# Optimization experiments

Hardware: AMD Instinct MI355X
Metric: run time of the kernel (lower is better)

Reference implementation:

```python
import jax, jax.numpy as jnp
import numpy as np

# model constants
D = 2048; D_INNER = 4096; H = 64; P = 64; N = 128; K = 4; CHUNK = 256
E = 8; TOPK = 2; I_EXP = 1024; I_SH = 4096
EPS = 1e-5; RES_MULT = 0.22
CONV_DIM = D_INNER + 2 * N  # n_groups=1


def rmsnorm(x, w, eps=EPS):
    var = jnp.mean(x * x, axis=-1, keepdims=True)
    return x * jax.lax.rsqrt(var + eps) * w


def segsum(x):
    # x: [..., L] -> [..., L, L] lower-triangular cumulative sums, -inf above diag
    L = x.shape[-1]
    cs = jnp.cumsum(x, axis=-1)
    d = cs[..., :, None] - cs[..., None, :]
    mask = jnp.tril(jnp.ones((L, L), dtype=bool))
    return jnp.where(mask, d, -jnp.inf)


def ssd(x, dt, A, Bm, Cm, chunk=CHUNK):
    # x:[b,s,h,p] dt:[b,s,h] A:[h] Bm/Cm:[b,s,n] (single group)
    b, S, h, p = x.shape
    n = Bm.shape[-1]
    nc = S // chunk
    xc = x.reshape(b, nc, chunk, h, p)
    dtc = dt.reshape(b, nc, chunk, h)
    Bc = Bm.reshape(b, nc, chunk, n)
    Cc = Cm.reshape(b, nc, chunk, n)
    dA = jnp.transpose(dtc * A, (0, 1, 3, 2))          # [b,c,h,l]
    dA_cum = jnp.cumsum(dA, axis=-1)                    # [b,c,h,l]
    xdt = xc * dtc[..., None]                           # [b,c,l,h,p]
    # intra-chunk (quadratic attention-like block)
    CB = jnp.einsum('bcln,bcsn->bcls', Cc, Bc)
    Lmat = jnp.exp(segsum(dA))                          # [b,c,h,l,s]
    Y = jnp.einsum('bcls,bchls,bcshp->bclhp', CB, Lmat, xdt)
    # per-chunk final states
    decay_states = jnp.exp(dA_cum[..., -1:] - dA_cum)   # [b,c,h,l]
    states = jnp.einsum('bcln,bchl,bclhp->bchpn', Bc, decay_states, xdt)
    # inter-chunk recurrence (small scan over nc chunks)
    chunk_decay = jnp.exp(dA_cum[..., -1])              # [b,c,h]
    dec_c = jnp.moveaxis(chunk_decay, 1, 0)             # [c,b,h]
    st_c = jnp.moveaxis(states, 1, 0)                   # [c,b,h,p,n]

    def step(carry, inp):
        dec, st = inp
        return carry * dec[..., None, None] + st, carry

    _, prev = jax.lax.scan(step, jnp.zeros_like(st_c[0]), (dec_c, st_c))
    prev = jnp.moveaxis(prev, 0, 1)                     # [b,c,h,p,n] state before each chunk
    out_decay = jnp.exp(jnp.transpose(dA_cum, (0, 1, 3, 2)))  # [b,c,l,h]
    Y = Y + jnp.einsum('bcln,bchpn->bclhp', Cc, prev) * out_decay[..., None]
    return Y.reshape(b, S, h, p)


def causal_conv_silu(u, w, bias):
    # u:[b,s,c], depthwise causal conv kernel w:[c,K]
    S = u.shape[1]
    up = jnp.pad(u, ((0, 0), (K - 1, 0), (0, 0)))
    y = sum(up[:, i:i + S, :] * w[:, i] for i in range(K)) + bias
    return jax.nn.silu(y)


def setup_inputs() -> dict:
    key = jax.random.key(0)
    ks = jax.random.split(key, 16)
    B, S = 1, 4096
    sc = 0.02
    return {
        'positions': jnp.arange(B * S, dtype=jnp.int32).reshape(B, S),
        'hidden_states': jax.random.normal(ks[0], (B, S, D), jnp.float32),
        'ln1_w': jnp.ones((D,), jnp.float32),
        'in_proj_w': jax.random.normal(ks[1], (D, 2 * D_INNER + 2 * N + H), jnp.float32) * sc,
        'conv_w': jax.random.normal(ks[2], (CONV_DIM, K), jnp.float32) * 0.2,
        'conv_b': jnp.zeros((CONV_DIM,), jnp.float32),
        'A_log': jnp.log(jax.random.uniform(ks[3], (H,), jnp.float32, 1.0, 16.0)),
        'dt_bias': jax.random.normal(ks[4], (H,), jnp.float32) * 0.5,
        'D_param': jnp.ones((H,), jnp.float32),
        'mamba_norm_w': jnp.ones((D_INNER,), jnp.float32),
        'out_proj_w': jax.random.normal(ks[5], (D_INNER, D), jnp.float32) * sc,
        'ln2_w': jnp.ones((D,), jnp.float32),
        'router_w': jax.random.normal(ks[6], (D, E), jnp.float32) * sc,
        'moe_w_gate_up': jax.random.normal(ks[7], (E, D, 2 * I_EXP), jnp.float32) * sc,
        'moe_w_down': jax.random.normal(ks[8], (E, I_EXP, D), jnp.float32) * sc,
        'shared_w_in': jax.random.normal(ks[9], (D, 2 * I_SH), jnp.float32) * sc,
        'shared_w_out': jax.random.normal(ks[10], (I_SH, D), jnp.float32) * sc,
    }


def reference(positions, hidden_states, ln1_w, in_proj_w, conv_w, conv_b, A_log,
              dt_bias, D_param, mamba_norm_w, out_proj_w, ln2_w, router_w,
              moe_w_gate_up, moe_w_down, shared_w_in, shared_w_out):
    B, S, _ = hidden_states.shape
    residual = hidden_states
    h = rmsnorm(hidden_states, ln1_w)
    # ---- Mamba2 mixer ----
    proj = h @ in_proj_w                                  # [B,S,2*Di+2N+H]
    z = proj[..., :D_INNER]
    xBC = proj[..., D_INNER:D_INNER + CONV_DIM]
    dt_raw = proj[..., D_INNER + CONV_DIM:]
    xBC = causal_conv_silu(xBC, conv_w, conv_b)
    x = xBC[..., :D_INNER].reshape(B, S, H, P)
    Bm = xBC[..., D_INNER:D_INNER + N]
    Cm = xBC[..., D_INNER + N:]
    dt = jax.nn.softplus(dt_raw + dt_bias)                # [B,S,H]
    A = -jnp.exp(A_log)                                   # [H]
    y = ssd(x, dt, A, Bm, Cm) + x * D_param[None, None, :, None]
    y = y.reshape(B, S, D_INNER)
    y = rmsnorm(y * jax.nn.silu(z), mamba_norm_w)         # gated RMSNorm
    mamba_out = y @ out_proj_w
    hidden = residual + mamba_out * RES_MULT
    residual = hidden
    # ---- MoE + shared MLP ----
    h2 = rmsnorm(hidden, ln2_w)
    ht = h2.reshape(-1, D)
    T = ht.shape[0]
    logits = ht @ router_w                                # [T,E]
    topv, topi = jax.lax.top_k(logits, TOPK)
    wts = jax.nn.softmax(topv, axis=-1)
    gates = jnp.zeros((T, E), ht.dtype).at[jnp.arange(T)[:, None], topi].set(wts)
    moe_out = jnp.zeros_like(ht)
    for e in range(E):
        gu = ht @ moe_w_gate_up[e]
        a = jax.nn.silu(gu[:, :I_EXP]) * gu[:, I_EXP:]
        moe_out = moe_out + gates[:, e:e + 1] * (a @ moe_w_down[e])
    gu = ht @ shared_w_in
    shared_out = (jax.nn.silu(gu[:, :I_SH]) * gu[:, I_SH:]) @ shared_w_out
    ff = (moe_out + shared_out).reshape(B, S, D)
    hidden = residual + ff * RES_MULT
    return (hidden, residual)
```

## Files before the change

### kernel.cpp

```cpp
#include <hip/hip_runtime.h>
#include <stdint.h>

typedef unsigned short u16;
typedef __attribute__((ext_vector_type(8))) __bf16 bf16x8;
typedef __attribute__((ext_vector_type(4))) float f32x4;

#define SEQ     4096
#define DMODEL  2048
#define DINNER  4096
#define NHEADS  64
#define HEADP   64
#define NSTATE  128
#define NCHUNK  16
#define CHUNKL  256
#define NPROJ   8512
#define NPROJP  8576
#define CONVDIM 4352
#define RESM    0.22f
#define MAXROWS 9216
#define MAXTILE 72

static __device__ __forceinline__ u16 f2bf(float f){
  union { float f; uint32_t u; } v; v.f = f;
  uint32_t r = v.u + 0x7fffu + ((v.u >> 16) & 1u);
// ... 248 lines not shown
      for (int i = 0; i < 4; i++) {
        const float v = acc[mi][ni][i];
        const float vp = __shfl_xor(v, 1);
        if (!(fr & 1)) {
          const int m = m0 + wr * 64 + mi * 16 + g * 4 + i;
          aout[(size_t)m * Nhalf + (n >> 1)] = f2bf(siluf(v) * vp);
        }
      }
    }
  }
}

template<int EPI>
__global__ __launch_bounds__(256, 2) void gemm_dd(
    const u16* __restrict__ Ah, const u16* __restrict__ Al,
    const u16* __restrict__ Bh, const u16* __restrict__ Bl,
    float* __restrict__ Cf, const float* __restrict__ res,
    int Nreal, int K, int ldc, float alpha, int NB, int MB, int G)
{
  __shared__ u16 Ash[128 * 32];
  __shared__ u16 Asl[128 * 32];
  __shared__ u16 Bsh[128 * 32];
  __shared__ u16 Bsl[128 * 32];
  int bx, by; decode_tile(blockIdx.x, NB, MB, G, bx, by);
  const int tid = threadIdx.x, lane = tid & 63;
  const int wid = tid >> 6, wr = wid >> 1, wc = wid & 1;
  const int m0 = by * 128, n0 = bx * 128;
  const int fr = lane & 15, g = lane >> 4;
  const int sl8 = swz_rd_sl8(fr, g);
  const f32x4 zero = {0.f, 0.f, 0.f, 0.f};
  f32x4 acc[4][4];
  #pragma unroll
  for (int i = 0; i < 4; i++)
    #pragma unroll
    for (int j = 0; j < 4; j++) acc[i][j] = zero;
  const int c8 = swz_src_c8(tid);
  const size_t offA = (size_t)(m0 + (tid >> 2)) * K + c8;
  const size_t offB = (size_t)(n0 + (tid >> 2)) * K + c8;
  const size_t rstep = (size_t)64 * K;
  const int l0 = tid * 8;
  for (int k0 = 0; k0 < K; k0 += 32) {
    if (k0) __syncthreads();
    gll16(Ah + offA + k0,         &Ash[l0]);
    gll16(Ah + offA + k0 + rstep, &Ash[2048 + l0]);
    gll16(Al + offA + k0,         &Asl[l0]);
    gll16(Al + offA + k0 + rstep, &Asl[2048 + l0]);
    gll16(Bh + offB + k0,         &Bsh[l0]);
    gll16(Bh + offB + k0 + rstep, &Bsh[2048 + l0]);
    gll16(Bl + offB + k0,         &Bsl[l0]);
    gll16(Bl + offB + k0 + rstep, &Bsl[2048 + l0]);
    __syncthreads();
    bf16x8 ah[4], al[4], bh[4], bl[4];
    #pragma unroll
    for (int mi = 0; mi < 4; mi++) {
      const int a = (wr * 64 + mi * 16 + fr) * 32 + sl8;
      ah[mi] = *(const bf16x8*)&Ash[a];
      al[mi] = *(const bf16x8*)&Asl[a];
    }
    #pragma unroll
    for (int ni = 0; ni < 4; ni++) {
      const int b = (wc * 64 + ni * 16 + fr) * 32 + sl8;
      bh[ni] = *(const bf16x8*)&Bsh[b];
      bl[ni] = *(const bf16x8*)&Bsl[b];
    }
    #pragma unroll
    for (int mi = 0; mi < 4; mi++)
      #pragma unroll
      for (int ni = 0; ni < 4; ni++) {
        acc[mi][ni] = __builtin_amdgcn_mfma_f32_16x16x32_bf16(al[mi], bh[ni], acc[mi][ni], 0, 0, 0);
        acc[mi][ni] = __builtin_amdgcn_mfma_f32_16x16x32_bf16(ah[mi], bl[ni], acc[mi][ni], 0, 0, 0);
        acc[mi][ni] = __builtin_amdgcn_mfma_f32_16x16x32_bf16(ah[mi], bh[ni], acc[mi][ni], 0, 0, 0);
      }
  }
  #pragma unroll
  for (int mi = 0; mi < 4; mi++) {
    #pragma unroll
    for (int ni = 0; ni < 4; ni++) {
      const int n = n0 + wc * 64 + ni * 16 + fr;
      if (n >= Nreal) continue;
      #pragma unroll
      for (int i = 0; i < 4; i++) {
        const int m = m0 + wr * 64 + mi * 16 + g * 4 + i;
        const float v = acc[mi][ni][i];
        const size_t idx = (size_t)m * ldc + n;
        if constexpr (EPI == 1) {
          Cf[idx] = res[idx] + alpha * v;
        } else {
          Cf[idx] = v;
        }
      }
    }
  }
}

__global__ __launch_bounds__(256, 2) void gemm_moe_gu(
    const u16* __restrict__ ht, const u16* __restrict__ wGU,
    u16* __restrict__ abufp, const int* __restrict__ tokmap,
    const int* __restrict__ meta)
{
  const int by = blockIdx.y;
  if (by >= meta[24]) return;
  const int e = meta[32 + by];
  const int row0 = meta[104 + by];
  __shared__ u16 As[128 * 32];
  __shared__ u16 Bs[128 * 32];
  const int tid = threadIdx.x, lane = tid & 63;
  const int wid = tid >> 6, wr = wid >> 1, wc = wid & 1;
  const int n0 = blockIdx.x * 128;
  const int fr = lane & 15, g = lane >> 4;
  const int sl8 = swz_rd_sl8(fr, g);
  const f32x4 zero = {0.f, 0.f, 0.f, 0.f};
  f32x4 acc[4][4];
  #pragma unroll
  for (int i = 0; i < 4; i++)
    #pragma unroll
    for (int j = 0; j < 4; j++) acc[i][j] = zero;
  const int r4 = tid >> 2, c8 = swz_src_c8(tid);
  const int tok0 = tokmap[row0 + r4];
  const int tok1 = tokmap[row0 + 64 + r4];
  const u16* pA0 = ht + (size_t)tok0 * DMODEL + c8;
  const u16* pA1 = ht + (size_t)tok1 * DMODEL + c8;
  const u16* pB  = wGU + (size_t)e * 2048 * DMODEL + (size_t)(n0 + r4) * DMODEL + c8;
  const size_t rstep = (size_t)64 * DMODEL;
  const int l0 = tid * 8;
  for (int k0 = 0; k0 < DMODEL; k0 += 32) {
    if (k0) __syncthreads();
    gll16(pA0 + k0,        &As[l0]);
    gll16(pA1 + k0,        &As[2048 + l0]);
    gll16(pB + k0,         &Bs[l0]);
    gll16(pB + k0 + rstep, &Bs[2048 + l0]);
    __syncthreads();
    bf16x8 af[4], bfr[4];
    #pragma unroll
    for (int mi = 0; mi < 4; mi++)
      af[mi] = *(const bf16x8*)&As[(wr * 64 + mi * 16 + fr) * 32 + sl8];
    #pragma unroll
    for (int ni = 0; ni < 4; ni++)
      bfr[ni] = *(const bf16x8*)&Bs[(wc * 64 + ni * 16 + fr) * 32 + sl8];
    #pragma unroll
    for (int mi = 0; mi < 4; mi++)
      #pragma unroll
      for (int ni = 0; ni < 4; ni++)
        acc[mi][ni] = __builtin_amdgcn_mfma_f32_16x16x32_bf16(af[mi], bfr[ni], acc[mi][ni], 0, 0, 0);
  }
  #pragma unroll
  for (int mi = 0; mi < 4; mi++)
    #pragma unroll
    for (int ni = 0; ni < 4; ni++) {
      const int n = n0 + wc * 64 + ni * 16 + fr;
      #pragma unroll
      for (int i = 0; i < 4; i++) {
        const float v = acc[mi][ni][i];
        const float vp = __shfl_xor(v, 1);
        if (!(fr & 1)) {
          const int m = row0 + wr * 64 + mi * 16 + g * 4 + i;
          abufp[(size_t)m * 1024 + (n >> 1)] = f2bf(siluf(v) * vp);
        }
      }
    }
}

__global__ __launch_bounds__(256, 2) void gemm_moe_down(
    const u16* __restrict__ abuf, const u16* __restrict__ wDN,
    u16* __restrict__ dout, const float* __restrict__ gatew,
    const int* __restrict__ meta)
{
  const int by = blockIdx.y;
  if (by >= meta[24]) return;
  const int e = meta[32 + by];
  const int row0 = meta[104 + by];
  __shared__ u16 As[128 * 32];
  __shared__ u16 Bs[128 * 32];
  const int tid = threadIdx.x, lane = tid & 63;
  const int wid = tid >> 6, wr = wid >> 1, wc = wid & 1;
  const int n0 = blockIdx.x * 128;
  const int fr = lane & 15, g = lane >> 4;
  const int sl8 = swz_rd_sl8(fr, g);
  const f32x4 zero = {0.f, 0.f, 0.f, 0.f};
  f32x4 acc[4][4];
  #pragma unroll
  for (int i = 0; i < 4; i++)
    #pragma unroll
    for (int j = 0; j < 4; j++) acc[i][j] = zero;
  const int r4 = tid >> 2, c8 = swz_src_c8(tid);
  const u16* pA = abuf + (size_t)(row0 + r4) * 1024 + c8;
  const u16* pB = wDN + (size_t)e * 1024 * 2048 + (size_t)(n0 + r4) * 1024 + c8;
  const size_t rstepA = (size_t)64 * 1024;
  const int l0 = tid * 8;
  for (int k0 = 0; k0 < 1024; k0 += 32) {
    if (k0) __syncthreads();
    gll16(pA + k0,          &As[l0]);
    gll16(pA + k0 + rstepA, &As[2048 + l0]);
    gll16(pB + k0,          &Bs[l0]);
    gll16(pB + k0 + rstepA, &Bs[2048 + l0]);
    __syncthreads();
    bf16x8 af[4], bfr[4];
    #pragma unroll
    for (int mi = 0; mi < 4; mi++)
      af[mi] = *(const bf16x8*)&As[(wr * 64 + mi * 16 + fr) * 32 + sl8];
    #pragma unroll
    for (int ni = 0; ni < 4; ni++)
      bfr[ni] = *(const bf16x8*)&Bs[(wc * 64 + ni * 16 + fr) * 32 + sl8];
    #pragma unroll
    for (int mi = 0; mi < 4; mi++)
      #pragma unroll
      for (int ni = 0; ni < 4; ni++)
        acc[mi][ni] = __builtin_amdgcn_mfma_f32_16x16x32_bf16(af[mi], bfr[ni], acc[mi][ni], 0, 0, 0);
  }
  #pragma unroll
  for (int mi = 0; mi < 4; mi++)
    #pragma unroll
    for (int ni = 0; ni < 4; ni++) {
      const int n = n0 + wc * 64 + ni * 16 + fr;
      #pragma unroll
      for (int i = 0; i < 4; i++) {
        const int m = row0 + wr * 64 + mi * 16 + g * 4 + i;
        dout[(size_t)m * 2048 + n] = f2bf(acc[mi][ni][i] * gatew[m]);
      }
    }
}

__global__ __launch_bounds__(256) void conv_silu_dt(
    const float* __restrict__ proj, const float* __restrict__ cw, const float* __restrict__ cb,
    const float* __restrict__ dt_bias,
    float* __restrict__ x, float* __restrict__ Bc, float* __restrict__ Cc,
    float* __restrict__ dt)
{
  const int c = blockIdx.x * 256 + threadIdx.x;
  const int s = blockIdx.y;
  if (c < CONVDIM) {
    const float4 w = *(const float4*)&cw[c * 4];
    float acc = cb[c];
    const float* pc = proj + (size_t)DINNER + c;
    if (s >= 3) acc += pc[(size_t)(s-3) * NPROJP] * w.x;
    if (s >= 2) acc += pc[(size_t)(s-2) * NPROJP] * w.y;
    if (s >= 1) acc += pc[(size_t)(s-1) * NPROJP] * w.z;
    acc += pc[(size_t)s * NPROJP] * w.w;
    const float v = siluf(acc);
    if (c < DINNER)                 x[(size_t)s * DINNER + c] = v;
    else if (c < DINNER + NSTATE)   Bc[(size_t)s * NSTATE + (c - DINNER)] = v;
    else                            Cc[(size_t)s * NSTATE + (c - DINNER - NSTATE)] = v;
  } else if (c < CONVDIM + 64) {
    const int h = c - CONVDIM;
    const float v = proj[(size_t)s * NPROJP + (DINNER + CONVDIM) + h] + dt_bias[h];
    dt[(size_t)s * 64 + h] = fmaxf(v, 0.f) + log1pf(__expf(-fabsf(v)));
  }
}

__global__ __launch_bounds__(64) void ssd_cum_seq(
    const float* __restrict__ dt, const float* __restrict__ A_log,
    float* __restrict__ cum, float* __restrict__ cdec)
{
  const int c = blockIdx.x, h = threadIdx.x;
  const float A = -__expf(A_log[h]);
  float run = 0.f;
  float* co = cum + ((size_t)(c * 64 + h)) * 256;
  const float* dp = dt + (size_t)c * 256 * 64 + h;
  #pragma unroll 4
  for (int l = 0; l < 256; l++) {
    run += dp[(size_t)l * 64] * A;
    co[l] = run;
  }
  cdec[c * 64 + h] = __expf(run);
}

__global__ __launch_bounds__(256) void ssd_cb(
    const float* __restrict__ Cc, const float* __restrict__ Bc, float* __restrict__ CBt)
{
  const int c = blockIdx.y;
  const int lt = blockIdx.x >> 2, st = blockIdx.x & 3;
  if (st > lt) return;
  __shared__ float Cn[128][64];
  __shared__ float Bn[128][64];
  const int tid = threadIdx.x;
  #pragma unroll
  for (int rep = 0; rep < 8; rep++) {
    const int lin = rep * 1024 + tid * 4;
    const int r = lin >> 7, cc = lin & 127;
    float4 cv = *(const float4*)&Cc[((size_t)(c*256 + lt*64 + r)) * 128 + cc];
    float4 bv = *(const float4*)&Bc[((size_t)(c*256 + st*64 + r)) * 128 + cc];
    Cn[cc+0][r] = cv.x; Cn[cc+1][r] = cv.y; Cn[cc+2][r] = cv.z; Cn[cc+3][r] = cv.w;
    Bn[cc+0][r] = bv.x; Bn[cc+1][r] = bv.y; Bn[cc+2][r] = bv.z; Bn[cc+3][r] = bv.w;
  }
  __syncthreads();
  const int lb = (tid >> 4) * 4, sb = (tid & 15) * 4;
  float acc[4][4] = {};
  for (int n = 0; n < 128; n++) {
    float cv[4], bv[4];
    #pragma unroll
    for (int i = 0; i < 4; i++) { cv[i] = Cn[n][lb+i]; bv[i] = Bn[n][sb+i]; }
    #pragma unroll
    for (int i = 0; i < 4; i++)
      #pragma unroll
      for (int j = 0; j < 4; j++) acc[i][j] += cv[i] * bv[j];
  }
  #pragma unroll
  for (int is = 0; is < 4; is++) {
    const int sg = st*64 + sb + is;
    float4 o; o.x = acc[0][is]; o.y = acc[1][is]; o.z = acc[2][is]; o.w = acc[3][is];
    *(float4*)&CBt[((size_t)(c*256 + sg)) * 256 + lt*64 + lb] = o;
  }
}

__global__ __launch_bounds__(256, 2) void ssd_intra(
    const float* __restrict__ x, const float* __restrict__ dt, const float* __restrict__ cum,
    const float* __restrict__ CBt, float* __restrict__ Yw)
{
  const int c = blockIdx.x, h = blockIdx.y, l = threadIdx.x;
  __shared__ float xs[64][64];
  __shared__ float cumL[256];
  cumL[l] = cum[((size_t)(c*64 + h)) * 256 + l];
  float Y[64];
  #pragma unroll
  for (int p = 0; p < 64; p++) Y[p] = 0.f;
  const size_t cb0 = (size_t)c * 256 * 256;
  for (int st4 = 0; st4 < 4; st4++) {
    __syncthreads();
    {
      const int j = threadIdx.x >> 2, p0 = (threadIdx.x & 3) * 16;
      const int sg = c*256 + st4*64 + j;
      const float dtv = dt[(size_t)sg * 64 + h];
      const float* xr = x + (size_t)sg * DINNER + h*64 + p0;
      #pragma unroll
      for (int q4 = 0; q4 < 4; q4++) {
        const float4 v = *(const float4*)&xr[q4*4];
        xs[j][p0 + q4*4+0] = v.x * dtv;
        xs[j][p0 + q4*4+1] = v.y * dtv;
        xs[j][p0 + q4*4+2] = v.z * dtv;
        xs[j][p0 + q4*4+3] = v.w * dtv;
      }
    }
    __syncthreads();
    if (st4 * 64 <= l) {
      const float myc = cumL[l];
      const int smax = (64 < l - st4*64 + 1) ? 64 : (l - st4*64 + 1);
      for (int s = 0; s < smax; s++) {
        const int sg = st4*64 + s;
        const float coef = CBt[cb0 + (size_t)sg*256 + l] * __expf(myc - cumL[sg]);
        const float4* xr4 = (const float4*)&xs[s][0];
        #pragma unroll
        for (int p4 = 0; p4 < 16; p4++) {
          const float4 xv = xr4[p4];
          Y[p4*4+0] += coef * xv.x;
          Y[p4*4+1] += coef * xv.y;
          Y[p4*4+2] += coef * xv.z;
          Y[p4*4+3] += coef * xv.w;
        }
      }
    }
  }
  float* yo = Yw + (size_t)(c*256 + l) * DINNER + h*64;
  #pragma unroll
  for (int p4 = 0; p4 < 16; p4++) {
    float4 o; o.x = Y[p4*4+0]; o.y = Y[p4*4+1]; o.z = Y[p4*4+2]; o.w = Y[p4*4+3];
    *(float4*)&yo[p4*4] = o;
  }
}

__global__ __launch_bounds__(256, 2) void ssd_states(
    const float* __restrict__ x, const float* __restrict__ Bc, const float* __restrict__ dt,
    const float* __restrict__ cum, float* __restrict__ states)
{
  const int c = blockIdx.x, h = blockIdx.y;
  const int p = threadIdx.x >> 2, n0 = (threadIdx.x & 3) * 32;
  __shared__ float xl[64][64];
  __shared__ float Bl[64][128];
  __shared__ float cd[256];
  {
    const int l = threadIdx.x;
    const float* cumh = cum + ((size_t)(c*64 + h)) * 256;
    cd[l] = __expf(cumh[255] - cumh[l]) * dt[(size_t)(c*256 + l) * 64 + h];
  }
  float stv[32];
  #pragma unroll
  for (int q = 0; q < 32; q++) stv[q] = 0.f;
  for (int lt = 0; lt < 4; lt++) {
    __syncthreads();
    {
      const int j = threadIdx.x >> 2, p0 = (threadIdx.x & 3) * 16;
      const int sg = c*256 + lt*64 + j;
      const float* xr = x + (size_t)sg * DINNER + h*64 + p0;
      #pragma unroll
      for (int q4 = 0; q4 < 4; q4++)
        *(float4*)&xl[j][p0 + q4*4] = *(const float4*)&xr[q4*4];
    }
    #pragma unroll
    for (int rep = 0; rep < 8; rep++) {
      const int lin = rep * 1024 + threadIdx.x * 4;
      const int r = lin >> 7, cc = lin & 127;
      *(float4*)&Bl[r][cc] = *(const float4*)&Bc[((size_t)(c*256 + lt*64 + r)) * 128 + cc];
    }
    __syncthreads();
    for (int j = 0; j < 64; j++) {
      const float v = xl[j][p] * cd[lt*64 + j];
      const float4* br = (const float4*)&Bl[j][n0];
      #pragma unroll
      for (int q4 = 0; q4 < 8; q4++) {
        const float4 bv = br[q4];
        stv[q4*4+0] += v * bv.x;
        stv[q4*4+1] += v * bv.y;
        stv[q4*4+2] += v * bv.z;
        stv[q4*4+3] += v * bv.w;
      }
    }
  }
  float* so = states + (((size_t)(c*64 + h)) * 64 + p) * 128 + n0;
  #pragma unroll
  for (int q4 = 0; q4 < 8; q4++) {
    float4 o; o.x = stv[q4*4+0]; o.y = stv[q4*4+1]; o.z = stv[q4*4+2]; o.w = stv[q4*4+3];
    *(float4*)&so[q4*4] = o;
  }
}

__global__ void ssd_scan(
    const float* __restrict__ states, const float* __restrict__ cdec, float* __restrict__ prev)
{
  const int hp = blockIdx.x;
  const int n = threadIdx.x;
  const int h = hp >> 6;
  float carry = 0.f;
  for (int c = 0; c < NCHUNK; c++) {
    const size_t idx = ((size_t)c * 4096 + hp) * 128 + n;
    prev[idx] = carry;
    carry = carry * cdec[c*64 + h] + states[idx];
  }
}

__global__ __launch_bounds__(256, 2) void ssd_final(
    const float* __restrict__ Cc, const float* __restrict__ prev, const float* __restrict__ cum,
    const float* __restrict__ x, const float* __restrict__ proj, const float* __restrict__ Dp,
    float* __restrict__ Yw)
{
  const int c = blockIdx.x, h = blockIdx.y, l = threadIdx.x;
  __shared__ float pv[64][128];
  #pragma unroll
  for (int rep = 0; rep < 8; rep++) {
    const int lin = rep * 1024 + threadIdx.x * 4;
    const int p = lin >> 7, n = lin & 127;
    *(float4*)&pv[p][n] = *(const float4*)&prev[((size_t)c * 4096 + h*64 + p) * 128 + n];
  }
  __syncthreads();
  float acc[64];
  #pragma unroll
  for (int p = 0; p < 64; p++) acc[p] = 0.f;
  const float* ccrow = Cc + (size_t)(c*256 + l) * 128;
  for (int nt = 0; nt < 4; nt++) {
    float cr[32];
    #pragma unroll
    for (int j4 = 0; j4 < 8; j4++) {
      const float4 v = *(const float4*)&ccrow[nt*32 + j4*4];
      cr[j4*4+0] = v.x; cr[j4*4+1] = v.y; cr[j4*4+2] = v.z; cr[j4*4+3] = v.w;
    }
    #pragma unroll
    for (int p = 0; p < 64; p++) {
      const float4* pvp = (const float4*)&pv[p][nt*32];
      float s = 0.f;
      #pragma unroll
      for (int j4 = 0; j4 < 8; j4++) {
        const float4 b = pvp[j4];
        s += cr[j4*4+0]*b.x + cr[j4*4+1]*b.y + cr[j4*4+2]*b.z + cr[j4*4+3]*b.w;
      }
      acc[p] += s;
    }
  }
  const float odec = __expf(cum[((size_t)(c*64 + h)) * 256 + l]);
  const float Dv = Dp[h];
  const float* xr = x + (size_t)(c*256 + l) * DINNER + h*64;
  const float* zr = proj + (size_t)(c*256 + l) * NPROJP + h*64;
  float* yo = Yw + (size_t)(c*256 + l) * DINNER + h*64;
  #pragma unroll
  for (int p = 0; p < 64; p++) {
    const float yv = yo[p] + acc[p] * odec + Dv * xr[p];
    yo[p] = yv * siluf(zr[p]);
  }
}

__global__ __launch_bounds__(256) void router_norm(
    const float* __restrict__ h2, const float* __restrict__ ln2w,
    const float* __restrict__ rw, u16* __restrict__ ht,
    int* __restrict__ eidx, float* __restrict__ ew)
{
  const int t = blockIdx.x;
  const float* xr = h2 + (size_t)t * DMODEL;
  float ss = 0.f;
  for (int i = threadIdx.x * 4; i < DMODEL; i += 1024) {
    float4 v = *(const float4*)&xr[i];
    ss += v.x*v.x + v.y*v.y + v.z*v.z + v.w*v.w;
  }
  #pragma unroll
  for (int off = 32; off > 0; off >>= 1) ss += __shfl_down(ss, off);
  __shared__ float red[4];
  if ((threadIdx.x & 63) == 0) red[threadIdx.x >> 6] = ss;
  __syncthreads();
  const float scale = rsqrtf((red[0]+red[1]+red[2]+red[3]) / (float)DMODEL + 1e-5f);
  float acc[8];
  #pragma unroll
  for (int j = 0; j < 8; j++) acc[j] = 0.f;
  u16* o = ht + (size_t)t * DMODEL;
  for (int i = threadIdx.x; i < DMODEL; i += 256) {
    const float v = xr[i] * scale * ln2w[i];
    o[i] = f2bf(v);
    const float* r = rw + (size_t)i * 8;
    #pragma unroll
    for (int j = 0; j < 8; j++) acc[j] += v * r[j];
  }
  #pragma unroll
  for (int j = 0; j < 8; j++)
    #pragma unroll
    for (int off = 32; off > 0; off >>= 1) acc[j] += __shfl_down(acc[j], off);
  __shared__ float rbuf[4][8];
  if ((threadIdx.x & 63) == 0)
    #pragma unroll
    for (int j = 0; j < 8; j++) rbuf[threadIdx.x >> 6][j] = acc[j];
  __syncthreads();
  if (threadIdx.x == 0) {
    float lg[8];
    #pragma unroll
    for (int j = 0; j < 8; j++) lg[j] = rbuf[0][j]+rbuf[1][j]+rbuf[2][j]+rbuf[3][j];
    int i1 = 0;
    #pragma unroll
    for (int j = 1; j < 8; j++) if (lg[j] > lg[i1]) i1 = j;
    int i2 = -1;
    #pragma unroll
    for (int j = 0; j < 8; j++) if (j != i1 && (i2 < 0 || lg[j] > lg[i2])) i2 = j;
    const float e2 = __expf(lg[i2] - lg[i1]);
    const float inv = 1.f / (1.f + e2);
    eidx[t*2]   = i1;  ew[t*2]   = inv;
    eidx[t*2+1] = i2;  ew[t*2+1] = e2 * inv;
  }
}

__global__ void moe_zero(int* __restrict__ tokmap, int* __restrict__ meta)
{
  const int i = blockIdx.x * 256 + threadIdx.x;
  if (i < MAXROWS) tokmap[i] = 0;
  if (i < 16) meta[i] = 0;
}

__global__ void moe_count(const int* __restrict__ eidx, int* __restrict__ meta)
{
  const int i = blockIdx.x * 256 + threadIdx.x;
  if (i < SEQ * 2) atomicAdd(&meta[eidx[i]], 1);
}

__global__ void moe_offsets(int* __restrict__ meta)
{
  if (threadIdx.x != 0 || blockIdx.x != 0) return;
  int off = 0, T = 0;
  for (int e = 0; e < 8; e++) {
    meta[16 + e] = off;
    const int nt = (meta[e] + 127) >> 7;
    for (int j = 0; j < nt; j++) {
      meta[32 + T] = e;
      meta[104 + T] = off + j * 128;
      T++;
    }
    off += nt * 128;
  }
  meta[24] = T;
}

__global__ void moe_place(
    const int* __restrict__ eidx, const float* __restrict__ ew,
    int* __restrict__ meta, int* __restrict__ tokmap,
    float* __restrict__ gatew, int* __restrict__ posmap)
{
  const int i = blockIdx.x * 256 + threadIdx.x;
  if (i >= SEQ * 2) return;
  const int e = eidx[i];
  const int pos = atomicAdd(&meta[8 + e], 1);
  const int r = meta[16 + e] + pos;
  tokmap[r] = i >> 1;
  gatew[r] = ew[i];
  posmap[i] = r;
}

__global__ __launch_bounds__(256) void final_moe(
    const float* __restrict__ h2, const float* __restrict__ shout,
    const u16* __restrict__ dout, const int* __restrict__ posmap,
    float* __restrict__ o)
{
  const int t = blockIdx.x;
  const int p0 = posmap[t*2], p1 = posmap[t*2+1];
  const u16* d0 = dout + (size_t)p0 * 2048 + threadIdx.x * 8;
  const u16* d1 = dout + (size_t)p1 * 2048 + threadIdx.x * 8;
  const size_t base = (size_t)t * 2048 + threadIdx.x * 8;
  #pragma unroll
  for (int q = 0; q < 8; q++) {
    const float ff = shout[base + q] + bf2f(d0[q]) + bf2f(d1[q]);
    o[base + q] = h2[base + q] + RESM * ff;
  }
}

#define OFF_WAH   ((size_t)0)
#define OFF_WAL   ((size_t)35127296)
#define OFF_PROJ  ((size_t)70254592)
#define OFF_X     ((size_t)210763776)
#define OFF_Y     ((size_t)277872640)
#define OFF_HP    ((size_t)344981504)
#define OFF_BC    ((size_t)378535936)
#define OFF_CC    ((size_t)380633088)
#define OFF_DT    ((size_t)382730240)
#define OFF_CUM   ((size_t)383778816)
#define OFF_CDEC  ((size_t)384827392)
#define OFF_CB    ((size_t)384831488)

extern "C" void kernel_launch(void* const* d_in, const int* in_sizes, int n_in,
                              void* d_out, int out_size, void* d_ws, size_t ws_size,
                              hipStream_t stream)
{
  const float* hs       = (const float*)d_in[1];
  const float* ln1_w    = (const float*)d_in[2];
  const float* w_inproj = (const float*)d_in[3];
  const float* conv_w   = (const float*)d_in[4];
  const float* conv_b   = (const float*)d_in[5];
  const float* A_log    = (const float*)d_in[6];
  const float* dt_bias  = (const float*)d_in[7];
  const float* D_param  = (const float*)d_in[8];
  const float* mnorm_w  = (const float*)d_in[9];
  const float* w_outp   = (const float*)d_in[10];
  const float* ln2_w    = (const float*)d_in[11];
  const float* router_w = (const float*)d_in[12];
  const float* w_gu     = (const float*)d_in[13];
  const float* w_down   = (const float*)d_in[14];
  const float* w_shin   = (const float*)d_in[15];
  const float* w_shout  = (const float*)d_in[16];

  char* ws = (char*)d_ws;
  u16*   wAh    = (u16*)(ws + OFF_WAH);
  u16*   wAl    = (u16*)(ws + OFF_WAL);
  float* projf  = (float*)(ws + OFF_PROJ);
  float* xbuf   = (float*)(ws + OFF_X);
  float* ybuf   = (float*)(ws + OFF_Y);
  float* Bcb    = (float*)(ws + OFF_BC);
  float* Ccb    = (float*)(ws + OFF_CC);
  float* dtb    = (float*)(ws + OFF_DT);
  float* cumb   = (float*)(ws + OFF_CUM);
  float* cdecb  = (float*)(ws + OFF_CDEC);
  float* cbt    = (float*)(ws + OFF_CB);

  u16*   hhi    = (u16*)(ws + OFF_HP);
  u16*   hlo    = (u16*)(ws + OFF_HP + 16777216);
  float* prevb  = (float*)(ws + OFF_HP);
  u16*   wDN    = (u16*)(ws + OFF_HP);
  float* stbuf  = (float*)(ws + OFF_WAH);
  u16*   ynhi   = (u16*)(ws + OFF_WAH);
  u16*   ynlo   = (u16*)(ws + OFF_WAL);
  u16*   wBh    = (u16*)(ws + OFF_PROJ);
  u16*   wBl    = (u16*)(ws + OFF_PROJ + 16777216);
  u16*   wE     = (u16*)(ws + OFF_WAH);
  u16*   wD     = (u16*)(ws + OFF_WAH + 33554432);
  u16*   wGU    = (u16*)(ws + OFF_WAH);
  u16*   abufp  = (u16*)(ws + OFF_PROJ + 83886080);
  u16*   ht     = (u16*)(ws + OFF_X);
  u16*   ash    = (u16*)(ws + OFF_X + 16777216);
  u16*   dout   = (u16*)(ws + OFF_X + 16777216);
  float* shout  = (float*)(ws + OFF_Y);

  int*   eidx   = (int*)(ws + OFF_BC);
  float* ew     = (float*)(ws + OFF_BC + 65536);
  int*   posmap = (int*)(ws + OFF_BC + 131072);
  int*   tokmap = (int*)(ws + OFF_BC + 196608);
  float* gatew  = (float*)(ws + OFF_BC + 262144);
  int*   meta   = (int*)(ws + OFF_BC + 327680);

  float* out0    = (float*)d_out;
  float* hidden2 = out0 + (size_t)SEQ * DMODEL;

  rmsnorm_split<<<SEQ, 256, 0, stream>>>(hs, ln1_w, hhi, hlo, DMODEL);
  wconv_t_split<<<dim3(NPROJ/32, DMODEL/32), 256, 0, stream>>>(w_inproj, wAh, wAl, DMODEL, NPROJ);
  gemm_dd<3><<<67*32, 256, 0, stream>>>(hhi, hlo, wAh, wAl, projf, nullptr,
                                        NPROJ, DMODEL, NPROJP, 0.f, 67, 32, 4);
  conv_silu_dt<<<dim3(18, SEQ), 256, 0, stream>>>(projf, conv_w, conv_b, dt_bias,
                                                  xbuf, Bcb, Ccb, dtb);
  ssd_cum_seq<<<NCHUNK, 64, 0, stream>>>(dtb, A_log, cumb, cdecb);
  ssd_cb<<<dim3(16, NCHUNK), 256, 0, stream>>>(Ccb, Bcb, cbt);
  ssd_intra<<<dim3(NCHUNK, NHEADS), 256, 0, stream>>>(xbuf, dtb, cumb, cbt, ybuf);
  ssd_states<<<dim3(NCHUNK, NHEADS), 256, 0, stream>>>(xbuf, Bcb, dtb, cumb, stbuf);
  ssd_scan<<<NHEADS*HEADP, 128, 0, stream>>>(stbuf, cdecb, prevb);
  ssd_final<<<dim3(NCHUNK, NHEADS), 256, 0, stream>>>(Ccb, prevb, cumb, xbuf, projf, D_param, ybuf);
  rmsnorm_split<<<SEQ, 256, 0, stream>>>(ybuf, mnorm_w, ynhi, ynlo, DINNER);
  wconv_t_split<<<dim3(DMODEL/32, DINNER/32), 256, 0, stream>>>(w_outp, wBh, wBl, DINNER, DMODEL);
  gemm_dd<1><<<16*32, 256, 0, stream>>>(ynhi, ynlo, wBh, wBl, hidden2, hs,
                                        DMODEL, DINNER, DMODEL, RESM, 16, 32, 4);

  router_norm<<<SEQ, 256, 0, stream>>>(hidden2, ln2_w, router_w, ht, eidx, ew);
  moe_zero<<<(MAXROWS+255)/256, 256, 0, stream>>>(tokmap, meta);
  moe_count<<<SEQ*2/256, 256, 0, stream>>>(eidx, meta);
  moe_offsets<<<1, 64, 0, stream>>>(meta);
  moe_place<<<SEQ*2/256, 256, 0, stream>>>(eidx, ew, meta, tokmap, gatew, posmap);

  wconv_t_glu<<<dim3(8192/32, DMODEL/32), 256, 0, stream>>>(w_shin, wE, DMODEL, 8192, 4096);
  gemm_bt_glu<<<64*32, 256, 0, stream>>>(ht, wE, ash, DMODEL, 4096, 64, 32, 4);
  wconv_t<<<dim3(DMODEL/32, 4096/32), 256, 0, stream>>>(w_shout, wD, 4096, DMODEL);
  gemm_bt<3><<<16*32, 256, 0, stream>>>(ash, wD, shout, DMODEL, 4096, DMODEL, 16, 32, 4);

  wconv_t_glu<<<dim3(2048/32, DMODEL/32, 8), 256, 0, stream>>>(w_gu, wGU, DMODEL, 2048, 1024);
  wconv_t<<<dim3(DMODEL/32, 1024/32, 8), 256, 0, stream>>>(w_down, wDN, 1024, DMODEL);
  gemm_moe_gu<<<dim3(16, MAXTILE), 256, 0, stream>>>(ht, wGU, abufp, tokmap, meta);
  gemm_moe_down<<<dim3(16, MAXTILE), 256, 0, stream>>>(abufp, wDN, dout, gatew, meta);

  final_moe<<<SEQ, 256, 0, stream>>>(hidden2, shout, dout, posmap, out0);
}
```

Before: 2.046 ms.

## Move SSD intra, states and final contractions onto split-bf16 MFMA

Result: faster. 1.806 ms (-11.8%).

```diff
diff --git a/kernel.cpp b/kernel.cpp
--- a/kernel.cpp
+++ b/kernel.cpp
@@ -574,114 +574,177 @@
   }
 }
 
-__global__ __launch_bounds__(256, 2) void ssd_intra(
+__global__ __launch_bounds__(256, 2) void ssd_intra_mfma(
     const float* __restrict__ x, const float* __restrict__ dt, const float* __restrict__ cum,
     const float* __restrict__ CBt, float* __restrict__ Yw)
 {
-  const int c = blockIdx.x, h = blockIdx.y, l = threadIdx.x;
-  __shared__ float xs[64][64];
+  const int c = blockIdx.x, h = blockIdx.y;
+  const int tid = threadIdx.x, lane = tid & 63, w = tid >> 6;
+  const int fr = lane & 15, g = lane >> 4;
   __shared__ float cumL[256];
-  cumL[l] = cum[((size_t)(c*64 + h)) * 256 + l];
-  float Y[64];
-  #pragma unroll
-  for (int p = 0; p < 64; p++) Y[p] = 0.f;
-  const size_t cb0 = (size_t)c * 256 * 256;
-  for (int st4 = 0; st4 < 4; st4++) {
+  __shared__ u16 Ph[256 * 32], Pl[256 * 32];
+  __shared__ u16 Xh[64 * 32],  Xl[64 * 32];
+  cumL[tid] = cum[((size_t)(c*64 + h)) * 256 + tid];
+  const f32x4 zero = {0.f, 0.f, 0.f, 0.f};
+  f32x4 acc[4][4];
+  #pragma unroll
+  for (int i = 0; i < 4; i++)
+    #pragma unroll
+    for (int j = 0; j < 4; j++) acc[i][j] = zero;
+  const size_t cb0 = (size_t)c * 65536;
+  for (int ts = 0; ts < 8; ts++) {
     __syncthreads();
     {
-      const int j = threadIdx.x >> 2, p0 = (threadIdx.x & 3) * 16;
-      const int sg = c*256 + st4*64 + j;
+      const int sl = tid >> 3, p0 = (tid & 7) * 8;
+      const int sg = c*256 + ts*32 + sl;
       const float dtv = dt[(size_t)sg * 64 + h];
       const float* xr = x + (size_t)sg * DINNER + h*64 + p0;
-      #pragma unroll
-      for (int q4 = 0; q4 < 4; q4++) {
-        const float4 v = *(const float4*)&xr[q4*4];
-        xs[j][p0 + q4*4+0] = v.x * dtv;
-        xs[j][p0 + q4*4+1] = v.y * dtv;
-        xs[j][p0 + q4*4+2] = v.z * dtv;
-        xs[j][p0 + q4*4+3] = v.w * dtv;
+      const float4 v0 = *(const float4*)&xr[0];
+      const float4 v1 = *(const float4*)&xr[4];
+      #pragma unroll
+      for (int q = 0; q < 8; q++) {
+        const float v = ((q < 4) ? ((const float*)&v0)[q] : ((const float*)&v1)[q-4]) * dtv;
+        const u16 H = f2bf(v);
+        Xh[(p0 + q) * 32 + sl] = H;
+        Xl[(p0 + q) * 32 + sl] = f2bf(v - bf2f(H));
+      }
+    }
+    {
+      const int l = tid;
+      const float myc = cumL[l];
+      #pragma unroll 4
+      for (int j = 0; j < 32; j++) {
+        const int s = ts*32 + j;
+        const float cb = CBt[cb0 + (size_t)s * 256 + l];
+        float p = 0.f;
+        if (s <= l) p = cb * __expf(myc - cumL[s]);
+        const u16 H = f2bf(p);
+        Ph[l * 32 + j] = H;
+        Pl[l * 32 + j] = f2bf(p - bf2f(H));
       }
     }
     __syncthreads();
-    if (st4 * 64 <= l) {
-      const float myc = cumL[l];
-      const int smax = (64 < l - st4*64 + 1) ? 64 : (l - st4*64 + 1);
-      for (int s = 0; s < smax; s++) {
-        const int sg = st4*64 + s;
-        const float coef = CBt[cb0 + (size_t)sg*256 + l] * __expf(myc - cumL[sg]);
-        const float4* xr4 = (const float4*)&xs[s][0];
+    if (ts * 32 < (w + 1) * 64) {
+      bf16x8 ah[4], al[4], bh[4], bl[4];
+      #pragma unroll
+      for (int mi = 0; mi < 4; mi++) {
+        const int a = (w*64 + mi*16 + fr) * 32 + g*8;
+        ah[mi] = *(const bf16x8*)&Ph[a];
+        al[mi] = *(const bf16x8*)&Pl[a];
+      }
+      #pragma unroll
+      for (int ni = 0; ni < 4; ni++) {
+        const int b = (ni*16 + fr) * 32 + g*8;
+        bh[ni] = *(const bf16x8*)&Xh[b];
+        bl[ni] = *(const bf16x8*)&Xl[b];
+      }
+      #pragma unroll
+      for (int mi = 0; mi < 4; mi++)
         #pragma unroll
-        for (int p4 = 0; p4 < 16; p4++) {
-          const float4 xv = xr4[p4];
-          Y[p4*4+0] += coef * xv.x;
-          Y[p4*4+1] += coef * xv.y;
-          Y[p4*4+2] += coef * xv.z;
-          Y[p4*4+3] += coef * xv.w;
+        for (int ni = 0; ni < 4; ni++) {
+          acc[mi][ni] = __builtin_amdgcn_mfma_f32_16x16x32_bf16(al[mi], bl[ni], acc[mi][ni], 0, 0, 0);
+          acc[mi][ni] = __builtin_amdgcn_mfma_f32_16x16x32_bf16(al[mi], bh[ni], acc[mi][ni], 0, 0, 0);
+          acc[mi][ni] = __builtin_amdgcn_mfma_f32_16x16x32_bf16(ah[mi], bl[ni], acc[mi][ni], 0, 0, 0);
+          acc[mi][ni] = __builtin_amdgcn_mfma_f32_16x16x32_bf16(ah[mi], bh[ni], acc[mi][ni], 0, 0, 0);
         }
-      }
-    }
-  }
-  float* yo = Yw + (size_t)(c*256 + l) * DINNER + h*64;
-  #pragma unroll
-  for (int p4 = 0; p4 < 16; p4++) {
-    float4 o; o.x = Y[p4*4+0]; o.y = Y[p4*4+1]; o.z = Y[p4*4+2]; o.w = Y[p4*4+3];
-    *(float4*)&yo[p4*4] = o;
-  }
-}
-
-__global__ __launch_bounds__(256, 2) void ssd_states(
+    }
+  }
+  #pragma unroll
+  for (int mi = 0; mi < 4; mi++)
+    #pragma unroll
+    for (int ni = 0; ni < 4; ni++)
+      #pragma unroll
+      for (int i = 0; i < 4; i++) {
+        const int l = w*64 + mi*16 + g*4 + i;
+        const int p = ni*16 + fr;
+        Yw[(size_t)(c*256 + l) * DINNER + h*64 + p] = acc[mi][ni][i];
+      }
+}
+
+__global__ __launch_bounds__(256, 2) void ssd_states_mfma(
     const float* __restrict__ x, const float* __restrict__ Bc, const float* __restrict__ dt,
     const float* __restrict__ cum, float* __restrict__ states)
 {
   const int c = blockIdx.x, h = blockIdx.y;
-  const int p = threadIdx.x >> 2, n0 = (threadIdx.x & 3) * 32;
-  __shared__ float xl[64][64];
-  __shared__ float Bl[64][128];
+  const int tid = threadIdx.x, lane = tid & 63, w = tid >> 6;
+  const int fr = lane & 15, g = lane >> 4;
   __shared__ float cd[256];
+  __shared__ u16 Xth[64 * 32],  Xtl[64 * 32];
+  __shared__ u16 Bth[128 * 32], Btl[128 * 32];
   {
-    const int l = threadIdx.x;
     const float* cumh = cum + ((size_t)(c*64 + h)) * 256;
-    cd[l] = __expf(cumh[255] - cumh[l]) * dt[(size_t)(c*256 + l) * 64 + h];
-  }
-  float stv[32];
-  #pragma unroll
-  for (int q = 0; q < 32; q++) stv[q] = 0.f;
-  for (int lt = 0; lt < 4; lt++) {
+    cd[tid] = __expf(cumh[255] - cumh[tid]) * dt[(size_t)(c*256 + tid) * 64 + h];
+  }
+  const f32x4 zero = {0.f, 0.f, 0.f, 0.f};
+  f32x4 acc[4][2];
+  #pragma unroll
+  for (int i = 0; i < 4; i++) { acc[i][0] = zero; acc[i][1] = zero; }
+  for (int lt = 0; lt < 8; lt++) {
     __syncthreads();
     {
-      const int j = threadIdx.x >> 2, p0 = (threadIdx.x & 3) * 16;
-      const int sg = c*256 + lt*64 + j;
-      const float* xr = x + (size_t)sg * DINNER + h*64 + p0;
-      #pragma unroll
-      for (int q4 = 0; q4 < 4; q4++)
-        *(float4*)&xl[j][p0 + q4*4] = *(const float4*)&xr[q4*4];
-    }
-    #pragma unroll
-    for (int rep = 0; rep < 8; rep++) {
-      const int lin = rep * 1024 + threadIdx.x * 4;
-      const int r = lin >> 7, cc = lin & 127;
-      *(float4*)&Bl[r][cc] = *(const float4*)&Bc[((size_t)(c*256 + lt*64 + r)) * 128 + cc];
+      const int ll = tid >> 3, p0 = (tid & 7) * 8;
+      const int lg = c*256 + lt*32 + ll;
+      const float cdv = cd[lt*32 + ll];
+      const float* xr = x + (size_t)lg * DINNER + h*64 + p0;
+      const float4 v0 = *(const float4*)&xr[0];
+      const float4 v1 = *(const float4*)&xr[4];
+      #pragma unroll
+      for (int q = 0; q < 8; q++) {
+        const float v = ((q < 4) ? ((const float*)&v0)[q] : ((const float*)&v1)[q-4]) * cdv;
+        const u16 H = f2bf(v);
+        Xth[(p0 + q) * 32 + ll] = H;
+        Xtl[(p0 + q) * 32 + ll] = f2bf(v - bf2f(H));
+      }
+    }
+    {
+      const int ll = tid >> 3, n0 = (tid & 7) * 16;
+      const float* br = Bc + (size_t)(c*256 + lt*32 + ll) * 128 + n0;
+      #pragma unroll
+      for (int q4 = 0; q4 < 4; q4++) {
+        const float4 bv = *(const float4*)&br[q4*4];
+        #pragma unroll
+        for (int q = 0; q < 4; q++) {
+          const float v = ((const float*)&bv)[q];
+          const u16 H = f2bf(v);
+          Bth[(n0 + q4*4 + q) * 32 + ll] = H;
+          Btl[(n0 + q4*4 + q) * 32 + ll] = f2bf(v - bf2f(H));
+        }
+      }
     }
     __syncthreads();
-    for (int j = 0; j < 64; j++) {
-      const float v = xl[j][p] * cd[lt*64 + j];
-      const float4* br = (const float4*)&Bl[j][n0];
-      #pragma unroll
-      for (int q4 = 0; q4 < 8; q4++) {
-        const float4 bv = br[q4];
-        stv[q4*4+0] += v * bv.x;
-        stv[q4*4+1] += v * bv.y;
-        stv[q4*4+2] += v * bv.z;
-        stv[q4*4+3] += v * bv.w;
-      }
-    }
-  }
-  float* so = states + (((size_t)(c*64 + h)) * 64 + p) * 128 + n0;
-  #pragma unroll
-  for (int q4 = 0; q4 < 8; q4++) {
-    float4 o; o.x = stv[q4*4+0]; o.y = stv[q4*4+1]; o.z = stv[q4*4+2]; o.w = stv[q4*4+3];
-    *(float4*)&so[q4*4] = o;
-  }
+    bf16x8 ah[4], al[4], bh[2], bl[2];
+    #pragma unroll
+    for (int mi = 0; mi < 4; mi++) {
+      const int a = (mi*16 + fr) * 32 + g*8;
+      ah[mi] = *(const bf16x8*)&Xth[a];
+      al[mi] = *(const bf16x8*)&Xtl[a];
+    }
+    #pragma unroll
+    for (int ni = 0; ni < 2; ni++) {
+      const int b = (w*32 + ni*16 + fr) * 32 + g*8;
+      bh[ni] = *(const bf16x8*)&Bth[b];
+      bl[ni] = *(const bf16x8*)&Btl[b];
+    }
+    #pragma unroll
+    for (int mi = 0; mi < 4; mi++)
+      #pragma unroll
+      for (int ni = 0; ni < 2; ni++) {
+        acc[mi][ni] = __builtin_amdgcn_mfma_f32_16x16x32_bf16(al[mi], bl[ni], acc[mi][ni], 0, 0, 0);
+        acc[mi][ni] = __builtin_amdgcn_mfma_f32_16x16x32_bf16(al[mi], bh[ni], acc[mi][ni], 0, 0, 0);
+        acc[mi][ni] = __builtin_amdgcn_mfma_f32_16x16x32_bf16(ah[mi], bl[ni], acc[mi][ni], 0, 0, 0);
+        acc[mi][ni] = __builtin_amdgcn_mfma_f32_16x16x32_bf16(ah[mi], bh[ni], acc[mi][ni], 0, 0, 0);
+      }
+  }
+  #pragma unroll
+  for (int mi = 0; mi < 4; mi++)
+    #pragma unroll
+    for (int ni = 0; ni < 2; ni++)
+      #pragma unroll
+      for (int i = 0; i < 4; i++) {
+        const int p = mi*16 + g*4 + i;
+        const int n = w*32 + ni*16 + fr;
+        states[(((size_t)(c*64 + h)) * 64 + p) * 128 + n] = acc[mi][ni][i];
+      }
 }
 
 __global__ void ssd_scan(
@@ -698,52 +761,91 @@
   }
 }
 
-__global__ __launch_bounds__(256, 2) void ssd_final(
+__global__ __launch_bounds__(256, 2) void ssd_final_mfma(
     const float* __restrict__ Cc, const float* __restrict__ prev, const float* __restrict__ cum,
     const float* __restrict__ x, const float* __restrict__ proj, const float* __restrict__ Dp,
     float* __restrict__ Yw)
 {
-  const int c = blockIdx.x, h = blockIdx.y, l = threadIdx.x;
-  __shared__ float pv[64][128];
-  #pragma unroll
-  for (int rep = 0; rep < 8; rep++) {
-    const int lin = rep * 1024 + threadIdx.x * 4;
-    const int p = lin >> 7, n = lin & 127;
-    *(float4*)&pv[p][n] = *(const float4*)&prev[((size_t)c * 4096 + h*64 + p) * 128 + n];
-  }
-  __syncthreads();
-  float acc[64];
-  #pragma unroll
-  for (int p = 0; p < 64; p++) acc[p] = 0.f;
-  const float* ccrow = Cc + (size_t)(c*256 + l) * 128;
+  const int c = blockIdx.x, h = blockIdx.y;
+  const int tid = threadIdx.x, lane = tid & 63, w = tid >> 6;
+  const int fr = lane & 15, g = lane >> 4;
+  __shared__ float cumL[256];
+  __shared__ u16 Ch[256 * 32], Cl[256 * 32];
+  __shared__ u16 Pvh[64 * 32], Pvl[64 * 32];
+  cumL[tid] = cum[((size_t)(c*64 + h)) * 256 + tid];
+  const f32x4 zero = {0.f, 0.f, 0.f, 0.f};
+  f32x4 acc[4][4];
+  #pragma unroll
+  for (int i = 0; i < 4; i++)
+    #pragma unroll
+    for (int j = 0; j < 4; j++) acc[i][j] = zero;
   for (int nt = 0; nt < 4; nt++) {
-    float cr[32];
-    #pragma unroll
-    for (int j4 = 0; j4 < 8; j4++) {
-      const float4 v = *(const float4*)&ccrow[nt*32 + j4*4];
-      cr[j4*4+0] = v.x; cr[j4*4+1] = v.y; cr[j4*4+2] = v.z; cr[j4*4+3] = v.w;
-    }
-    #pragma unroll
-    for (int p = 0; p < 64; p++) {
-      const float4* pvp = (const float4*)&pv[p][nt*32];
-      float s = 0.f;
-      #pragma unroll
-      for (int j4 = 0; j4 < 8; j4++) {
-        const float4 b = pvp[j4];
-        s += cr[j4*4+0]*b.x + cr[j4*4+1]*b.y + cr[j4*4+2]*b.z + cr[j4*4+3]*b.w;
-      }
-      acc[p] += s;
-    }
-  }
-  const float odec = __expf(cum[((size_t)(c*64 + h)) * 256 + l]);
+    __syncthreads();
+    {
+      #pragma unroll
+      for (int rep = 0; rep < 32; rep++) {
+        const int l = rep*8 + (tid >> 5);
+        const int j = tid & 31;
+        const float v = Cc[(size_t)(c*256 + l) * 128 + nt*32 + j];
+        const u16 H = f2bf(v);
+        Ch[l*32 + j] = H;
+        Cl[l*32 + j] = f2bf(v - bf2f(H));
+      }
+    }
+    {
+      const int p = tid >> 2, q0 = (tid & 3) * 8;
+      const float* pr = prev + ((size_t)c * 4096 + h*64 + p) * 128 + nt*32 + q0;
+      const float4 v0 = *(const float4*)&pr[0];
+      const float4 v1 = *(const float4*)&pr[4];
+      #pragma unroll
+      for (int q = 0; q < 8; q++) {
+        const float v = (q < 4) ? ((const float*)&v0)[q] : ((const float*)&v1)[q-4];
+        const u16 H = f2bf(v);
+        Pvh[p*32 + q0 + q] = H;
+        Pvl[p*32 + q0 + q] = f2bf(v - bf2f(H));
+      }
+    }
+    __syncthreads();
+    bf16x8 ah[4], al[4], bh[4], bl[4];
+    #pragma unroll
+    for (int mi = 0; mi < 4; mi++) {
+      const int a = (w*64 + mi*16 + fr) * 32 + g*8;
+      ah[mi] = *(const bf16x8*)&Ch[a];
+      al[mi] = *(const bf16x8*)&Cl[a];
+    }
+    #pragma unroll
+    for (int ni = 0; ni < 4; ni++) {
+      const int b = (ni*16 + fr) * 32 + g*8;
+      bh[ni] = *(const bf16x8*)&Pvh[b];
+      bl[ni] = *(const bf16x8*)&Pvl[b];
+    }
+    #pragma unroll
+    for (int mi = 0; mi < 4; mi++)
+      #pragma unroll
+      for (int ni = 0; ni < 4; ni++) {
+        acc[mi][ni] = __builtin_amdgcn_mfma_f32_16x16x32_bf16(al[mi], bl[ni], acc[mi][ni], 0, 0, 0);
+        acc[mi][ni] = __builtin_amdgcn_mfma_f32_16x16x32_bf16(al[mi], bh[ni], acc[mi][ni], 0, 0, 0);
+        acc[mi][ni] = __builtin_amdgcn_mfma_f32_16x16x32_bf16(ah[mi], bl[ni], acc[mi][ni], 0, 0, 0);
+        acc[mi][ni] = __builtin_amdgcn_mfma_f32_16x16x32_bf16(ah[mi], bh[ni], acc[mi][ni], 0, 0, 0);
+      }
+  }
   const float Dv = Dp[h];
-  const float* xr = x + (size_t)(c*256 + l) * DINNER + h*64;
-  const float* zr = proj + (size_t)(c*256 + l) * NPROJP + h*64;
-  float* yo = Yw + (size_t)(c*256 + l) * DINNER + h*64;
-  #pragma unroll
-  for (int p = 0; p < 64; p++) {
-    const float yv = yo[p] + acc[p] * odec + Dv * xr[p];
-    yo[p] = yv * siluf(zr[p]);
+  #pragma unroll
+  for (int mi = 0; mi < 4; mi++) {
+    #pragma unroll
+    for (int i = 0; i < 4; i++) {
+      const int l = w*64 + mi*16 + g*4 + i;
+      const float odec = __expf(cumL[l]);
+      const size_t rowo = (size_t)(c*256 + l);
+      #pragma unroll
+      for (int ni = 0; ni < 4; ni++) {
+        const int p = ni*16 + fr;
+        const size_t iy = rowo * DINNER + h*64 + p;
+        const float yv = Yw[iy] + acc[mi][ni][i] * odec + Dv * x[iy];
+        const float z = proj[rowo * NPROJP + h*64 + p];
+        Yw[iy] = yv * siluf(z);
+      }
+    }
   }
 }
 
@@ -947,10 +1049,10 @@
                                                   xbuf, Bcb, Ccb, dtb);
   ssd_cum_seq<<<NCHUNK, 64, 0, stream>>>(dtb, A_log, cumb, cdecb);
   ssd_cb<<<dim3(16, NCHUNK), 256, 0, stream>>>(Ccb, Bcb, cbt);
-  ssd_intra<<<dim3(NCHUNK, NHEADS), 256, 0, stream>>>(xbuf, dtb, cumb, cbt, ybuf);
-  ssd_states<<<dim3(NCHUNK, NHEADS), 256, 0, stream>>>(xbuf, Bcb, dtb, cumb, stbuf);
+  ssd_intra_mfma<<<dim3(NCHUNK, NHEADS), 256, 0, stream>>>(xbuf, dtb, cumb, cbt, ybuf);
+  ssd_states_mfma<<<dim3(NCHUNK, NHEADS), 256, 0, stream>>>(xbuf, Bcb, dtb, cumb, stbuf);
   ssd_scan<<<NHEADS*HEADP, 128, 0, stream>>>(stbuf, cdecb, prevb);
-  ssd_final<<<dim3(NCHUNK, NHEADS), 256, 0, stream>>>(Ccb, prevb, cumb, xbuf, projf, D_param, ybuf);
+  ssd_final_mfma<<<dim3(NCHUNK, NHEADS), 256, 0, stream>>>(Ccb, prevb, cumb, xbuf, projf, D_param, ybuf);
   rmsnorm_split<<<SEQ, 256, 0, stream>>>(ybuf, mnorm_w, ynhi, ynlo, DINNER);
   wconv_t_split<<<dim3(DMODEL/32, DINNER/32), 256, 0, stream>>>(w_outp, wBh, wBl, DINNER, DMODEL);
   gemm_dd<1><<<16*32, 256, 0, stream>>>(ynhi, ynlo, wBh, wBl, hidden2, hs,
```
